# Optimization experiments

Measured on AMD Instinct MI355X. Metric: run time of the kernel, lower is better.

The kernel has to match this reference:

```python
import jax, jax.numpy as jnp
import numpy as np

N, E, R = 100000, 1600000, 64
DIN, DREL, DOUT, H = 32, 32, 64, 8
DH = DOUT // H


def setup_inputs() -> dict:
    key = jax.random.key(0)
    ks = jax.random.split(key, 10)
    emb_ent = jax.random.normal(ks[0], (N, DIN), dtype=jnp.float32)
    emb_rel = jax.random.normal(ks[1], (R, DREL), dtype=jnp.float32)
    attn_W = jax.random.normal(ks[2], (DOUT, 2 * DIN + DREL), dtype=jnp.float32) * 0.1
    attn_b = jnp.zeros((DOUT,), dtype=jnp.float32)
    attn_vec = jax.random.normal(ks[3], (1, H, DH), dtype=jnp.float32) * 0.1
    aggr_W = jax.random.normal(ks[4], (DOUT, DIN + DREL), dtype=jnp.float32) * 0.1
    aggr_b = jnp.zeros((DOUT,), dtype=jnp.float32)
    head_idxs = jax.random.randint(ks[5], (E,), 0, N, dtype=jnp.int32)
    # guarantee every node has at least one incoming edge (well-formed graph)
    tail_idxs = jnp.concatenate([
        jnp.arange(N, dtype=jnp.int32),
        jax.random.randint(ks[6], (E - N,), 0, N, dtype=jnp.int32),
    ])
    rel_idxs = jax.random.randint(ks[7], (E,), 0, R, dtype=jnp.int32)
    return {"emb_ent": emb_ent, "emb_rel": emb_rel, "attn_W": attn_W,
            "attn_b": attn_b, "attn_vec": attn_vec, "aggr_W": aggr_W,
            "aggr_b": aggr_b, "head_idxs": head_idxs, "tail_idxs": tail_idxs,
            "rel_idxs": rel_idxs}


def reference(emb_ent, emb_rel, attn_W, attn_b, attn_vec, aggr_W, aggr_b,
              head_idxs, tail_idxs, rel_idxs):
    num_ent = emb_ent.shape[0]
    # mean incoming relation embedding per entity (self-loop relation)
    edge_rel = emb_rel[rel_idxs]                                   # [E, Drel]
    ent_freq = jax.ops.segment_sum(jnp.ones_like(tail_idxs, dtype=edge_rel.dtype),
                                   tail_idxs, num_segments=num_ent)[:, None]
    self_rel = jax.ops.segment_sum(edge_rel, tail_idxs, num_segments=num_ent) / ent_freq
    # append self-loops
    emb_rels = jnp.concatenate([edge_rel, self_rel], axis=0)       # [E+N, Drel]
    loop = jnp.arange(num_ent, dtype=head_idxs.dtype)
    head = jnp.concatenate([head_idxs, loop])                      # [E+N]
    tail = jnp.concatenate([tail_idxs, loop])                      # [E+N]
    ent_tail = emb_ent[tail]
    ent_head = emb_ent[head]
    # attention logits per edge per head
    cat_att = jnp.concatenate([ent_tail, ent_head, emb_rels], axis=-1)  # [E+N, 2*Din+Drel]
    proj = jax.nn.leaky_relu(cat_att @ attn_W.T + attn_b, negative_slope=0.2)
    proj = proj.reshape(-1, H, DH)
    attn_raw = jnp.sum(proj * attn_vec, axis=-1, keepdims=True)    # [E+N, H, 1]
    # segment-softmax over incoming edges of each tail node
    amax = jax.ops.segment_max(attn_raw, tail, num_segments=num_ent)
    attn_val = jnp.exp(attn_raw - amax[tail])
    attn_sum = jax.ops.segment_sum(attn_val, tail, num_segments=num_ent)
    beta = attn_val / (attn_sum[tail] + 1e-16)                     # [E+N, H, 1]
    # weighted message aggregation
    cat_msg = jnp.concatenate([ent_head, emb_rels], axis=-1)       # [E+N, Din+Drel]
    msg = (cat_msg @ aggr_W.T + aggr_b).reshape(-1, H, DH)
    out = jax.ops.segment_sum(beta * msg, tail, num_segments=num_ent)  # [N, H, DH]
    return out.reshape(num_ent, H * DH)
```

## Files before the change

kernel.cpp:

```cpp
#include <hip/hip_runtime.h>
#include <math.h>

#define DIN 32
#define DREL 32
#define CATA 96
#define CATM 64
#define LOG2E 1.44269504088896340736f
#define MAXD 64

#define SCAT_B 2048
#define ART_B 16
#define ENT_B 512

__device__ __forceinline__ ushort f2bf(float x) {
  unsigned u = __float_as_uint(x);
  return (ushort)((u + 0x7FFFu + ((u >> 16) & 1u)) >> 16);
}
__device__ __forceinline__ float bf2f(ushort x) {
  return __uint_as_float(((unsigned)x) << 16);
}

__device__ __forceinline__ float fexp2(float x) {
#if __has_builtin(__builtin_amdgcn_exp2f)
  return __builtin_amdgcn_exp2f(x);
#else
  return __expf(x * 0.6931471805599453f);
#endif
}

__global__ __launch_bounds__(256) void k1_kernel(
    const float* __restrict__ emb_ent, const float* __restrict__ emb_rel,
    const float* __restrict__ attn_W, const float* __restrict__ aggr_W,
    const int* __restrict__ head_idxs, const int* __restrict__ tail_idxs,
    const int* __restrict__ rel_idxs,
    int* __restrict__ cnt16, int* __restrict__ emeta, float2* __restrict__ ART,
    ushort* __restrict__ A_tail, ushort* __restrict__ A_head, ushort* __restrict__ M_ent,
    int N, int R, int E) {
  int b = blockIdx.x;
  if (b < SCAT_B) {
    int tid = b * 256 + threadIdx.x;
    for (int e = tid; e < E; e += SCAT_B * 256) {
      int t = tail_idxs[e];
      int slot = atomicAdd(&cnt16[t << 4], 1);
      if (slot < MAXD)
        emeta[((size_t)t << 6) + slot] = (head_idxs[e] << 8) | rel_idxs[e];
    }
  } else if (b < SCAT_B + ART_B) {
    int i = (b - SCAT_B) * 256 + threadIdx.x;
    if (i < R * 64) {
      int r = i >> 6, o = i & 63;
      const float* er = emb_rel + r * DREL;
      float a = 0.f, t = 0.f;
#pragma unroll
      for (int k = 0; k < DREL; ++k) {
        float e = er[k];
        a = fmaf(attn_W[o * CATA + 2 * DIN + k], e, a);
        t = fmaf(aggr_W[o * CATM + DIN + k], e, t);
      }
      ART[i] = make_float2(a, t);
    }
  } else {
    int rb = b - SCAT_B - ART_B;
    int role = rb / ENT_B;
    int eb = rb - role * ENT_B;
    int lane = threadIdx.x & 63;
    int wid = __builtin_amdgcn_readfirstlane((int)((eb * 256 + threadIdx.x) >> 6));
    const int NW = ENT_B * 4;
    const float* wsrc = (role == 0) ? (attn_W + lane * CATA)
                      : (role == 1) ? (attn_W + lane * CATA + DIN)
                                    : (aggr_W + lane * CATM);
    ushort* dst = (role == 0) ? A_tail : (role == 1) ? A_head : M_ent;
    float w[DIN];
#pragma unroll
    for (int k = 0; k < DIN; ++k) w[k] = wsrc[k];
    for (int n = wid; n < N; n += NW) {
      const float* ent = emb_ent + (size_t)n * DIN;
      float d = 0.f;
#pragma unroll
      for (int k = 0; k < DIN; ++k) d = fmaf(w[k], ent[k], d);
      dst[((size_t)n << 6) + lane] = f2bf(d);
    }
  }
}

__global__ __launch_bounds__(256) void node_agg_kernel(
    const ushort* __restrict__ A_tail, const ushort* __restrict__ A_head,
    const ushort* __restrict__ M_ent, const float2* __restrict__ ART,
    const float* __restrict__ attn_b, const float* __restrict__ attn_vec,
    const float* __restrict__ aggr_b,
    const int* __restrict__ emeta, const int* __restrict__ cnt16,
    float* __restrict__ out, int N, int totalWaves) {
  int wid = __builtin_amdgcn_readfirstlane((int)((blockIdx.x * blockDim.x + threadIdx.x) >> 6));
  int lane = threadIdx.x & 63;
  float avec = attn_vec[lane] * LOG2E;
  float ab = attn_b[lane];
  float gb = aggr_b[lane];

  for (int t = wid; t < N; t += totalWaves) {
    int len = cnt16[t << 4];
    if (len > MAXD) len = MAXD;
    const int* ebase = emeta + ((size_t)t << 6);
    float at = bf2f(A_tail[((size_t)t << 6) + lane]) + ab;
    float m0 = -INFINITY, s0 = 0.f, a0 = 0.f;
    float m1 = -INFINITY, s1 = 0.f, a1 = 0.f;
    float suma = 0.f, sumt = 0.f;
    for (int base = 0; base < len; base += 64) {
      int nch = len - base; if (nch > 64) nch = 64;
      int sel = lane < nch ? lane : nch - 1;
      int mload = ebase[base + sel];
      int i = 0;
      for (; i + 2 <= nch; i += 2) {
        int mmA = __builtin_amdgcn_readlane(mload, i);
        int mmB = __builtin_amdgcn_readlane(mload, i + 1);
        int hnA = mmA >> 8, rA = mmA & 255;
        int hnB = mmB >> 8, rB = mmB & 255;
        float ahA = bf2f(A_head[((size_t)hnA << 6) + lane]);
        float meA = bf2f(M_ent[((size_t)hnA << 6) + lane]);
        float2 rtA = ART[(rA << 6) + lane];
        float ahB = bf2f(A_head[((size_t)hnB << 6) + lane]);
        float meB = bf2f(M_ent[((size_t)hnB << 6) + lane]);
        float2 rtB = ART[(rB << 6) + lane];
        suma += rtA.x + rtB.x;
        sumt += rtA.y + rtB.y;
        float preA = at + ahA + rtA.x;
        float vA = fmaxf(preA, 0.2f * preA) * avec;
        vA += __shfl_xor(vA, 1); vA += __shfl_xor(vA, 2); vA += __shfl_xor(vA, 4);
        float preB = at + ahB + rtB.x;
        float vB = fmaxf(preB, 0.2f * preB) * avec;
        vB += __shfl_xor(vB, 1); vB += __shfl_xor(vB, 2); vB += __shfl_xor(vB, 4);
        float mn0 = fmaxf(m0, vA);
        float c0 = fexp2(m0 - mn0), e0 = fexp2(vA - mn0);
        s0 = fmaf(s0, c0, e0);
        a0 = fmaf(a0, c0, e0 * (meA + rtA.y));
        m0 = mn0;
        float mn1 = fmaxf(m1, vB);
        float c1 = fexp2(m1 - mn1), e1 = fexp2(vB - mn1);
        s1 = fmaf(s1, c1, e1);
        a1 = fmaf(a1, c1, e1 * (meB + rtB.y));
        m1 = mn1;
      }
      if (i < nch) {
        int mm = __builtin_amdgcn_readlane(mload, i);
        int hn = mm >> 8, r = mm & 255;
        float ah = bf2f(A_head[((size_t)hn << 6) + lane]);
        float me = bf2f(M_ent[((size_t)hn << 6) + lane]);
        float2 rt = ART[(r << 6) + lane];
        suma += rt.x;
        sumt += rt.y;
        float pre = at + ah + rt.x;
        float v = fmaxf(pre, 0.2f * pre) * avec;
        v += __shfl_xor(v, 1); v += __shfl_xor(v, 2); v += __shfl_xor(v, 4);
        float mn0 = fmaxf(m0, v);
        float c0 = fexp2(m0 - mn0), e0 = fexp2(v - mn0);
        s0 = fmaf(s0, c0, e0);
        a0 = fmaf(a0, c0, e0 * (me + rt.y));
        m0 = mn0;
      }
    }
    float m = fmaxf(m0, m1);
    float c0 = fexp2(m0 - m), c1 = fexp2(m1 - m);
    float s = fmaf(s0, c0, s1 * c1);
    float acc = fmaf(a0, c0, a1 * c1);
    float invd = 1.f / (float)len;
    float ah = bf2f(A_head[((size_t)t << 6) + lane]);
    float me = bf2f(M_ent[((size_t)t << 6) + lane]);
    float pre = at + ah + suma * invd;
    float v = fmaxf(pre, 0.2f * pre) * avec;
    v += __shfl_xor(v, 1); v += __shfl_xor(v, 2); v += __shfl_xor(v, 4);
    float mn = fmaxf(m, v);
    float c = fexp2(m - mn);
    float e = fexp2(v - mn);
    s = fmaf(s, c, e);
    acc = fmaf(acc, c, e * (me + sumt * invd));
    out[((size_t)t << 6) + lane] = acc / (s + 1e-16f) + gb;
  }
}

extern "C" void kernel_launch(void* const* d_in, const int* in_sizes, int n_in,
                              void* d_out, int out_size, void* d_ws, size_t ws_size,
                              hipStream_t stream) {
  const float* emb_ent  = (const float*)d_in[0];
  const float* emb_rel  = (const float*)d_in[1];
  const float* attn_W   = (const float*)d_in[2];
  const float* attn_b   = (const float*)d_in[3];
  const float* attn_vec = (const float*)d_in[4];
  const float* aggr_W   = (const float*)d_in[5];
  const float* aggr_b   = (const float*)d_in[6];
  const int* head_idxs  = (const int*)d_in[7];
  const int* tail_idxs  = (const int*)d_in[8];
  const int* rel_idxs   = (const int*)d_in[9];

  const int N = in_sizes[0] / DIN;
  const int R = in_sizes[1] / DREL;
  const int E = in_sizes[7];
  float* out = (float*)d_out;

  char* ws = (char*)d_ws;
  size_t off = 0;
  int* cnt16 = (int*)(ws + off); off += (size_t)N * 16 * sizeof(int);
  int* emeta = (int*)(ws + off); off += (size_t)N * MAXD * sizeof(int);
  ushort* A_tail = (ushort*)(ws + off); off += (size_t)N * 64 * sizeof(ushort);
  ushort* A_head = (ushort*)(ws + off); off += (size_t)N * 64 * sizeof(ushort);
  ushort* M_ent  = (ushort*)(ws + off); off += (size_t)N * 64 * sizeof(ushort);
  float2* ART = (float2*)(ws + off); off += (size_t)R * 64 * sizeof(float2);

  hipMemsetAsync(cnt16, 0, (size_t)N * 16 * sizeof(int), stream);

  k1_kernel<<<SCAT_B + ART_B + 3 * ENT_B, 256, 0, stream>>>(
      emb_ent, emb_rel, attn_W, aggr_W, head_idxs, tail_idxs, rel_idxs,
      cnt16, emeta, ART, A_tail, A_head, M_ent, N, R, E);
  const int NB = 2048;
  node_agg_kernel<<<NB, 256, 0, stream>>>(A_tail, A_head, M_ent, ART,
                                          attn_b, attn_vec, aggr_b,
                                          emeta, cnt16, out, N, NB * 4);
}
```

Baseline: 331.8 us.

## Inline per-node edge counter into emeta row and split scatter kernel

Moves the per-node atomic counter into slot 0 of each node's 64-int emeta row, removing the separate cnt16 array. Edge records are now written with nontemporal stores. The fused k1 kernel is split into a separate scatter kernel and an entity/relation projection kernel. This drops a separate counter load in the aggregation kernel and shares a cache line between the count and its edges. The cost is memsetting the whole 25.6MB emeta buffer instead of a 6.4MB counter array, and capacity drops to 63 edges per node.

```diff
diff --git a/kernel.cpp b/kernel.cpp
--- a/kernel.cpp
+++ b/kernel.cpp
@@ -28,25 +28,28 @@
 #endif
 }
 
-__global__ __launch_bounds__(256) void k1_kernel(
+__global__ __launch_bounds__(256) void scat_kernel(
+    const int* __restrict__ head_idxs, const int* __restrict__ tail_idxs,
+    const int* __restrict__ rel_idxs, int* __restrict__ emeta, int E) {
+  int tid = blockIdx.x * 256 + threadIdx.x;
+  for (int e = tid; e < E; e += SCAT_B * 256) {
+    int t = tail_idxs[e];
+    int slot = atomicAdd(&emeta[(size_t)t << 6], 1) + 1;
+    if (slot < MAXD)
+      __builtin_nontemporal_store((head_idxs[e] << 8) | rel_idxs[e],
+                                  &emeta[((size_t)t << 6) + slot]);
+  }
+}
+
+__global__ __launch_bounds__(256) void entart_kernel(
     const float* __restrict__ emb_ent, const float* __restrict__ emb_rel,
     const float* __restrict__ attn_W, const float* __restrict__ aggr_W,
-    const int* __restrict__ head_idxs, const int* __restrict__ tail_idxs,
-    const int* __restrict__ rel_idxs,
-    int* __restrict__ cnt16, int* __restrict__ emeta, float2* __restrict__ ART,
+    float2* __restrict__ ART,
     ushort* __restrict__ A_tail, ushort* __restrict__ A_head, ushort* __restrict__ M_ent,
-    int N, int R, int E) {
+    int N, int R) {
   int b = blockIdx.x;
-  if (b < SCAT_B) {
-    int tid = b * 256 + threadIdx.x;
-    for (int e = tid; e < E; e += SCAT_B * 256) {
-      int t = tail_idxs[e];
-      int slot = atomicAdd(&cnt16[t << 4], 1);
-      if (slot < MAXD)
-        emeta[((size_t)t << 6) + slot] = (head_idxs[e] << 8) | rel_idxs[e];
-    }
-  } else if (b < SCAT_B + ART_B) {
-    int i = (b - SCAT_B) * 256 + threadIdx.x;
+  if (b < ART_B) {
+    int i = b * 256 + threadIdx.x;
     if (i < R * 64) {
       int r = i >> 6, o = i & 63;
       const float* er = emb_rel + r * DREL;
@@ -60,7 +63,7 @@
       ART[i] = make_float2(a, t);
     }
   } else {
-    int rb = b - SCAT_B - ART_B;
+    int rb = b - ART_B;
     int role = rb / ENT_B;
     int eb = rb - role * ENT_B;
     int lane = threadIdx.x & 63;
@@ -88,7 +91,7 @@
     const ushort* __restrict__ M_ent, const float2* __restrict__ ART,
     const float* __restrict__ attn_b, const float* __restrict__ attn_vec,
     const float* __restrict__ aggr_b,
-    const int* __restrict__ emeta, const int* __restrict__ cnt16,
+    const int* __restrict__ emeta,
     float* __restrict__ out, int N, int totalWaves) {
   int wid = __builtin_amdgcn_readfirstlane((int)((blockIdx.x * blockDim.x + threadIdx.x) >> 6));
   int lane = threadIdx.x & 63;
@@ -97,9 +100,9 @@
   float gb = aggr_b[lane];
 
   for (int t = wid; t < N; t += totalWaves) {
-    int len = cnt16[t << 4];
-    if (len > MAXD) len = MAXD;
     const int* ebase = emeta + ((size_t)t << 6);
+    int len = ebase[0];
+    if (len > MAXD - 1) len = MAXD - 1;
     float at = bf2f(A_tail[((size_t)t << 6) + lane]) + ab;
     float m0 = -INFINITY, s0 = 0.f, a0 = 0.f;
     float m1 = -INFINITY, s1 = 0.f, a1 = 0.f;
@@ -107,7 +110,7 @@
     for (int base = 0; base < len; base += 64) {
       int nch = len - base; if (nch > 64) nch = 64;
       int sel = lane < nch ? lane : nch - 1;
-      int mload = ebase[base + sel];
+      int mload = ebase[1 + base + sel];
       int i = 0;
       for (; i + 2 <= nch; i += 2) {
         int mmA = __builtin_amdgcn_readlane(mload, i);
@@ -197,20 +200,19 @@
 
   char* ws = (char*)d_ws;
   size_t off = 0;
-  int* cnt16 = (int*)(ws + off); off += (size_t)N * 16 * sizeof(int);
   int* emeta = (int*)(ws + off); off += (size_t)N * MAXD * sizeof(int);
   ushort* A_tail = (ushort*)(ws + off); off += (size_t)N * 64 * sizeof(ushort);
   ushort* A_head = (ushort*)(ws + off); off += (size_t)N * 64 * sizeof(ushort);
   ushort* M_ent  = (ushort*)(ws + off); off += (size_t)N * 64 * sizeof(ushort);
   float2* ART = (float2*)(ws + off); off += (size_t)R * 64 * sizeof(float2);
 
-  hipMemsetAsync(cnt16, 0, (size_t)N * 16 * sizeof(int), stream);
-
-  k1_kernel<<<SCAT_B + ART_B + 3 * ENT_B, 256, 0, stream>>>(
-      emb_ent, emb_rel, attn_W, aggr_W, head_idxs, tail_idxs, rel_idxs,
-      cnt16, emeta, ART, A_tail, A_head, M_ent, N, R, E);
+  hipMemsetAsync(emeta, 0, (size_t)N * MAXD * sizeof(int), stream);
+
+  scat_kernel<<<SCAT_B, 256, 0, stream>>>(head_idxs, tail_idxs, rel_idxs, emeta, E);
+  entart_kernel<<<ART_B + 3 * ENT_B, 256, 0, stream>>>(
+      emb_ent, emb_rel, attn_W, aggr_W, ART, A_tail, A_head, M_ent, N, R);
   const int NB = 2048;
   node_agg_kernel<<<NB, 256, 0, stream>>>(A_tail, A_head, M_ent, ART,
                                           attn_b, attn_vec, aggr_b,
-                                          emeta, cnt16, out, N, NB * 4);
-}
+                                          emeta, out, N, NB * 4);
+}
```

New measurement: 347.8 us. 4.8% more time.
